# Optimization experiments

Hardware: AMD Instinct MI355X
Metric: run time of the kernel (lower is better)

## Reference

```python
import jax, jax.numpy as jnp
import numpy as np

B, N, D, H, R = 4, 4096, 1024, 16, 64
HD = D // H  # head_dim = 64


def setup_inputs() -> dict:
    key = jax.random.key(0)
    ks = jax.random.split(key, 8)
    x = jax.random.normal(ks[0], (B, N, D), dtype=jnp.float32)
    # nn.Linear weights are (out, in); y = x @ W.T
    Wq = jax.random.normal(ks[1], (D, D), dtype=jnp.float32) * (1.0 / np.sqrt(D))
    Wk = jax.random.normal(ks[2], (D, D), dtype=jnp.float32) * (1.0 / np.sqrt(D))
    Wv = jax.random.normal(ks[3], (D, D), dtype=jnp.float32) * (1.0 / np.sqrt(D))
    Wo = jax.random.normal(ks[4], (D, D), dtype=jnp.float32) * (1.0 / np.sqrt(D))
    bo = jnp.zeros((D,), dtype=jnp.float32)
    E = jax.random.normal(ks[5], (N, R), dtype=jnp.float32) * 0.02
    Fm = jax.random.normal(ks[6], (N, R), dtype=jnp.float32) * 0.02
    return {"x": x, "Wq": Wq, "Wk": Wk, "Wv": Wv, "Wo": Wo, "bo": bo, "E": E, "Fm": Fm}


def reference(x, Wq, Wk, Wv, Wo, bo, E, Fm):
    b, n, d = x.shape
    scale = np.sqrt(HD).astype(np.float32)
    # projections: torch Linear => x @ W.T ; reshape to (B, H, N, HD)
    def proj(W):
        y = jnp.einsum('bnd,ed->bne', x, W)
        return y.reshape(b, n, H, HD).transpose(0, 2, 1, 3)
    Q = proj(Wq)  # (B,H,N,HD)
    K = proj(Wk)
    V = proj(Wv)
    # low-rank projections along sequence: (B,H,R,HD)
    K_low = jnp.einsum('nr,bhnd->bhrd', E[:n], K)
    V_low = jnp.einsum('nr,bhnd->bhrd', Fm[:n], V)
    scores = jnp.einsum('bhnd,bhrd->bhnr', Q, K_low) / scale  # (B,H,N,R)
    attn = jax.nn.softmax(scores, axis=-1)
    out = jnp.einsum('bhnr,bhrd->bhnd', attn, V_low)  # (B,H,N,HD)
    out = out.transpose(0, 2, 1, 3).reshape(b, n, d)
    return jnp.einsum('bnd,ed->bne', out, Wo) + bo
```

## Files before the change

### kernel.cpp

```cpp
#include <hip/hip_runtime.h>
#include <stdint.h>

typedef __bf16 bf16;
typedef __bf16 bf16x8 __attribute__((ext_vector_type(8)));
typedef __bf16 bf16x4 __attribute__((ext_vector_type(4)));
typedef float  f32x4  __attribute__((ext_vector_type(4)));

#define NB   4096
#define DB   1024
#define RV   64
#define MB   16384
#define NSEG 8

__global__ void detect_dtype(const unsigned short* x, int* flag) {
  __shared__ int cnt;
  if (threadIdx.x == 0) cnt = 0;
  __syncthreads();
  int local = 0;
  for (int i = threadIdx.x; i < 8192; i += 256) {
    const int e = (x[i] >> 7) & 0xFF;
    if (e >= 0xC0) local++;
  }
  atomicAdd(&cnt, local);
  __syncthreads();
  if (threadIdx.x == 0) *flag = (cnt > 64) ? 1 : 0;
}

struct CvtArgs {
  const void* src[8];
  bf16* dst[8];
  int n[8];
  int off[9];
};
__global__ void to_bf16_multi(CvtArgs a, const int* __restrict__ flag) {
  const int blk = blockIdx.x;
  int seg = 0;
#pragma unroll
  for (int s = 1; s < 8; ++s) seg += (blk >= a.off[s]);
  const int i = (blk - a.off[seg]) * 2048 + threadIdx.x * 8;
  if (i >= a.n[seg]) return;
  bf16* dst = a.dst[seg];
  if (*flag) {
    const float* s = (const float*)a.src[seg] + i;
    f32x4 x0 = *(const f32x4*)s;
    f32x4 x1 = *(const f32x4*)(s + 4);
    bf16x8 v;
    v[0]=(bf16)x0[0]; v[1]=(bf16)x0[1]; v[2]=(bf16)x0[2]; v[3]=(bf16)x0[3];
    v[4]=(bf16)x1[0]; v[5]=(bf16)x1[1]; v[6]=(bf16)x1[2]; v[7]=(bf16)x1[3];
    *(bf16x8*)(dst + i) = v;
  } else {
    *(uint4*)(dst + i) = *(const uint4*)((const bf16*)a.src[seg] + i);
  }
}

__global__ __launch_bounds__(256) void ef_transpose(
    const void* __restrict__ E, const void* __restrict__ F,
    bf16* __restrict__ EFt, const int* __restrict__ flag) {
  const int m = blockIdx.x;
  const int z = m >> 6, r = m & 63;
  const void* src = z ? F : E;
  const int t = threadIdx.x;
  bf16* dst = EFt + (size_t)m * 4096;
  if (*flag) {
    const float* s = (const float*)src;
#pragma unroll
    for (int i = 0; i < 16; ++i) {
      const int n = i*256 + t;
      dst[n] = (bf16)s[(size_t)n*RV + r];
    }
  } else {
    const bf16* s = (const bf16*)src;
#pragma unroll
    for (int i = 0; i < 16; ++i) {
      const int n = i*256 + t;
      dst[n] = s[(size_t)n*RV + r];
    }
  }
}

typedef __attribute__((address_space(1))) const void g_as1_void;
typedef __attribute__((address_space(3))) void as3_void;
static __device__ __forceinline__ void gload16(const void* g, void* l) {
  __builtin_amdgcn_global_load_lds((g_as1_void*)g, (as3_void*)l, 16, 0, 0);
}

__global__ __launch_bounds__(256, 4) void lowrank_mfma(
    const bf16* __restrict__ EFt, const bf16* __restrict__ xb,
    float* __restrict__ Pf) {
  const int b = blockIdx.x, dt = blockIdx.y, seg = blockIdx.z;
  __shared__ __align__(16) bf16 sEF0[128*64];
  __shared__ __align__(16) bf16 sEF1[128*64];
  __shared__ __align__(16) bf16 sXT[32*64];
  const int t = threadIdx.x, lane = t & 63, w = t >> 6;
  const int lr = lane & 15, quad = lane >> 4;
  const int wm = (w & 1) * 64, wd = (w >> 1) * 16;
  const int nbase = seg * (NB / NSEG);

  const bf16* gA[4];
  int abase[4];
#pragma unroll
  for (int i = 0; i < 4; ++i) {
    const int c = i*256 + t, row = c >> 3, ch = c & 7;
    gA[i] = EFt + (size_t)row*4096 + nbase + (ch ^ (row & 7))*8;
    abase[i] = (i*256 + (w << 6)) * 8;
  }
  const bf16* gx = xb + ((size_t)b*NB + nbase + lane)*DB + dt*32 + w*8;
  int xslot[8];
#pragma unroll
  for (int j = 0; j < 8; ++j) {
    const int d = w*8 + j;
    xslot[j] = (d*8 + ((lane >> 3) ^ (d & 7)))*8 + (lane & 7);
  }
  f32x4 acc[4] = {};

  uint4 rx = *(const uint4*)gx;
#pragma unroll
  for (int i = 0; i < 4; ++i) gload16(gA[i], sEF0 + abase[i]);
  asm volatile("s_waitcnt vmcnt(0)" ::: "memory");
  __syncthreads();

  for (int kt = 0; kt < NB/NSEG; kt += 64) {
    {
      const bf16* px = (const bf16*)&rx;
#pragma unroll
      for (int j = 0; j < 8; ++j) sXT[xslot[j]] = px[j];
    }
    bf16* nbuf = ((kt >> 6) & 1) ? sEF0 : sEF1;
    if (kt + 64 < NB/NSEG) {
#pragma unroll
      for (int i = 0; i < 4; ++i) gload16(gA[i] + kt + 64, nbuf + abase[i]);
      rx = *(const uint4*)(gx + (size_t)(kt + 64)*DB);
    }
    asm volatile("s_waitcnt lgkmcnt(0)" ::: "memory");
    __syncthreads();
    const bf16* cbuf = ((kt >> 6) & 1) ? sEF1 : sEF0;
#pragma unroll
    for (int ks = 0; ks < 2; ++ks) {
      const int kc = ks*4 + quad;
      const int dd = wd + lr;
      bf16x8 bv = *(const bf16x8*)(sXT + (dd*8 + (kc ^ (dd & 7)))*8);
#pragma unroll
      for (int mi = 0; mi < 4; ++mi) {
        const int m = wm + mi*16 + lr;
        bf16x8 af = *(const bf16x8*)(cbuf + (m*8 + (kc ^ (m & 7)))*8);
        acc[mi] = __builtin_amdgcn_mfma_f32_16x16x32_bf16(af, bv, acc[mi], 0, 0, 0);
      }
    }
    if (kt + 64 < NB/NSEG) asm volatile("s_waitcnt vmcnt(1)" ::: "memory");
    __syncthreads();
  }

  float* dst = Pf + (((size_t)seg*4 + b)*128)*DB + dt*32 + wd + lr;
#pragma unroll
  for (int mi = 0; mi < 4; ++mi) {
    const int row128 = wm + mi*16 + quad*4;
#pragma unroll
    for (int rg = 0; rg < 4; ++rg)
      dst[(size_t)(row128 + rg)*DB] = acc[mi][rg];
  }
}

__global__ __launch_bounds__(256) void lowrank_reduce(
    const float* __restrict__ Pf, bf16* __restrict__ xEb, bf16* __restrict__ xFb) {
  const int idx = blockIdx.x*256 + threadIdx.x;
  const int d4  = idx & 255;
  const int row = (idx >> 8) & 127;
  const int b   = idx >> 15;
  const float* p = Pf + ((size_t)b*128 + row)*DB + d4*4;
  f32x4 s = {};
#pragma unroll
  for (int seg = 0; seg < NSEG; ++seg) {
    f32x4 v = *(const f32x4*)(p + (size_t)seg*4*128*DB);
    s[0]+=v[0]; s[1]+=v[1]; s[2]+=v[2]; s[3]+=v[3];
  }
  bf16x4 o;
  o[0]=(bf16)s[0]; o[1]=(bf16)s[1]; o[2]=(bf16)s[2]; o[3]=(bf16)s[3];
  bf16* dst = (row < 64 ? xEb : xFb) + ((size_t)b*64 + (row & 63))*DB + d4*4;
  *(bf16x4*)dst = o;
}

struct GemmArgs {
  const bf16* A;
  const bf16* B;
  void* C;
  const bf16* bias;
  const int* oflag;
  int force_f32;
  int M, N, K;
  const bf16* A2;
  const bf16* B2;
  void* C2;
  int dual;
};

__global__ __launch_bounds__(512, 2) void gemm_nt(GemmArgs args) {
  const int K = args.K, N = args.N;
  const bf16* Aptr = args.A;
  const bf16* Bptr = args.B;
  void* Cptr = args.C;
  __shared__ __align__(16) char smem[131072];
  bf16* const sA[4] = {(bf16*)smem,           (bf16*)(smem + 32768),
                       (bf16*)(smem + 65536), (bf16*)(smem + 98304)};
  bf16* const sB[4] = {(bf16*)(smem + 16384), (bf16*)(smem + 49152),
                       (bf16*)(smem + 81920), (bf16*)(smem + 114688)};

  const int t = threadIdx.x;
  const int lane = t & 63;
  const int w = t >> 6;
  const int lr = lane & 15;
  const int quad = lane >> 4;
  const int wm = (w >> 2) * 128;
  const int wn = (w & 3) * 64;

  int bx = blockIdx.x, by = blockIdx.y;
  if (args.dual) {
    if (by == 1) { Aptr = args.A2; Bptr = args.B2; Cptr = args.C2; }
    by = 0;
  } else if (gridDim.y == 64) {
    const int l = by * 4 + bx;
    const int xcd = l & 7, s = l >> 3;
    by = xcd * 8 + (s >> 2);
    bx = s & 3;
  }
  const int m0 = by * 256;
  const int n0 = bx * 256;

  const bf16* gA[2];
  const bf16* gB[2];
  int lds_off[2];
#pragma unroll
  for (int i = 0; i < 2; ++i) {
    const int c = i*512 + t, row = c >> 2, ch = c & 3;
    const int sc = ch ^ ((row >> 1) & 3);
    gA[i] = Aptr + (size_t)(m0 + row)*K + sc*8;
    gB[i] = Bptr + (size_t)(n0 + row)*K + sc*8;
    lds_off[i] = c * 8;
  }
  auto stage = [&](bf16* dA, bf16* dB, int ko) {
#pragma unroll
    for (int i = 0; i < 2; ++i) gload16(gA[i] + ko, dA + lds_off[i]);
#pragma unroll
    for (int i = 0; i < 2; ++i) gload16(gB[i] + ko, dB + lds_off[i]);
  };

  f32x4 acc[8][4] = {};

#define GSUB(J, WS, DOSTAGE) do {                                            \
    asm volatile("s_waitcnt " WS ::: "memory");                              \
    __builtin_amdgcn_s_barrier();                                            \
    bf16x8 af[8], bv[4];                                                     \
    _Pragma("unroll")                                                        \
    for (int mi = 0; mi < 8; ++mi) {                                         \
      const int m = wm + mi*16 + lr;                                         \
      af[mi] = *(const bf16x8*)(sA[J] + m*32 + ((quad ^ ((m>>1)&3))*8));     \
    }                                                                        \
    _Pragma("unroll")                                                        \
    for (int ni = 0; ni < 4; ++ni) {                                         \
      const int n = wn + ni*16 + lr;                                         \
      bv[ni] = *(const bf16x8*)(sB[J] + n*32 + ((quad ^ ((n>>1)&3))*8));     \
    }                                                                        \
    if (DOSTAGE) stage(sA[((J)+3)&3], sB[((J)+3)&3], kt + ((J)+3)*32);       \
    __builtin_amdgcn_s_setprio(1);                                           \
    _Pragma("unroll")                                                        \
    for (int mi = 0; mi < 8; ++mi)                                           \
      _Pragma("unroll")                                                      \
      for (int ni = 0; ni < 4; ++ni)                                         \
        acc[mi][ni] = __builtin_amdgcn_mfma_f32_16x16x32_bf16(               \
            af[mi], bv[ni], acc[mi][ni], 0, 0, 0);                           \
    __builtin_amdgcn_s_setprio(0);                                           \
  } while (0)

  stage(sA[0], sB[0], 0);
  stage(sA[1], sB[1], 32);
  stage(sA[2], sB[2], 64);

  int kt = 0;
  for (; kt + 128 < K; kt += 128) {
    GSUB(0, "vmcnt(8)", 1);
    GSUB(1, "vmcnt(8)", 1);
    GSUB(2, "vmcnt(8)", 1);
    GSUB(3, "vmcnt(8)", 1);
  }
  GSUB(0, "vmcnt(8)", 1);
  GSUB(1, "vmcnt(8)", 0);
  GSUB(2, "vmcnt(4)", 0);
  GSUB(3, "vmcnt(0)", 0);
#undef GSUB

  __syncthreads();

  const int f32out = args.force_f32 | (args.oflag ? *args.oflag : 0);
  float* sEw = (float*)(smem + w * 16384);
#pragma unroll
  for (int h = 0; h < 2; ++h) {
    if (h) asm volatile("s_waitcnt lgkmcnt(0)" ::: "memory");
#pragma unroll
    for (int mi = 0; mi < 4; ++mi) {
#pragma unroll
      for (int ni = 0; ni < 4; ++ni) {
        const int colg = n0 + wn + ni*16 + lr;
        const float bvv = args.bias ? (float)args.bias[colg] : 0.0f;
#pragma unroll
        for (int rg = 0; rg < 4; ++rg) {
          const int row = mi*16 + quad*4 + rg;
          sEw[row*64 + ((ni*16 + lr) ^ ((row & 15)*4))] = acc[h*4 + mi][ni][rg] + bvv;
        }
      }
    }
    asm volatile("s_waitcnt lgkmcnt(0)" ::: "memory");
#pragma unroll
    for (int i = 0; i < 8; ++i) {
      const int c = i*64 + lane;
      const int row = c >> 3, ch = c & 7;
      const int d0 = ch * 8;
      const int swz = (row & 15) * 4;
      f32x4 v0 = *(const f32x4*)(sEw + row*64 + (d0 ^ swz));
      f32x4 v1 = *(const f32x4*)(sEw + row*64 + ((d0 + 4) ^ swz));
      const size_t base = (size_t)(m0 + wm + h*64 + row)*N + n0 + wn + d0;
      if (f32out) {
        *(f32x4*)((float*)Cptr + base)     = v0;
        *(f32x4*)((float*)Cptr + base + 4) = v1;
      } else {
        bf16x8 wv;
        wv[0]=(bf16)v0[0]; wv[1]=(bf16)v0[1]; wv[2]=(bf16)v0[2]; wv[3]=(bf16)v0[3];
        wv[4]=(bf16)v1[0]; wv[5]=(bf16)v1[1]; wv[6]=(bf16)v1[2]; wv[7]=(bf16)v1[3];
        *(bf16x8*)((bf16*)Cptr + base) = wv;
      }
    }
  }
}

__global__ __launch_bounds__(256, 2) void attn_mfma(
    const bf16* Q, const float* __restrict__ Klow,
    const float* __restrict__ Vlow, bf16* AO) {
  const int bh = blockIdx.x, b = bh >> 4, h = bh & 15;
  const int n0 = blockIdx.y * 128;

  __shared__ bf16 sQ[128*64];
  __shared__ bf16 sKb[64*64];
  __shared__ bf16 sVt[64*64];
  __shared__ bf16 sP[4][32*64];

  const int t = threadIdx.x;
  const int lane = t & 63;
  const int w = t >> 6;
  const int lr = lane & 15;
  const int quad = lane >> 4;

#pragma unroll
  for (int i = 0; i < 4; ++i) {
    const int c = i*256 + t;
    const int row = c >> 3, j = c & 7;
    const uint4 v = *(const uint4*)(Q + ((size_t)b*NB + n0 + row)*DB + h*64 + j*8);
    *(uint4*)(sQ + (row*8 + (j ^ (row & 7)))*8) = v;
  }
  {
    const int r = t >> 2, c0 = (t & 3) * 16;
    const float* kb = Klow + (size_t)(b*64 + r)*DB + h*64 + c0;
    const float* vb = Vlow + (size_t)(b*64 + r)*DB + h*64 + c0;
    float kf[16], vf[16];
#pragma unroll
    for (int i = 0; i < 4; ++i) {
      *(f32x4*)(kf + i*4) = *(const f32x4*)(kb + i*4);
      *(f32x4*)(vf + i*4) = *(const f32x4*)(vb + i*4);
    }
#pragma unroll
    for (int cc = 0; cc < 2; ++cc) {
      bf16x8 pk;
#pragma unroll
      for (int j2 = 0; j2 < 8; ++j2) pk[j2] = (bf16)kf[cc*8 + j2];
      const int ch = (c0 >> 3) + cc;
      *(bf16x8*)(sKb + (r*8 + (ch ^ (r & 7)))*8) = pk;
    }
#pragma unroll
    for (int j2 = 0; j2 < 16; ++j2) {
      const int d = c0 + j2;
      sVt[d*64 + (((r >> 3) ^ (d & 7))*8) + (r & 7)] = (bf16)vf[j2];
    }
  }
  __syncthreads();

  f32x4 accS[2][4] = {};
#pragma unroll
  for (int ks = 0; ks < 2; ++ks) {
    const int kc = ks*4 + quad;
    bf16x8 af[2], bv[4];
#pragma unroll
    for (int mi = 0; mi < 2; ++mi) {
      const int m = w*32 + mi*16 + lr;
      af[mi] = *(const bf16x8*)(sQ + (m*8 + (kc ^ (m & 7)))*8);
    }
#pragma unroll
    for (int ni = 0; ni < 4; ++ni) {
      const int r = ni*16 + lr;
      bv[ni] = *(const bf16x8*)(sKb + (r*8 + (kc ^ (r & 7)))*8);
    }
#pragma unroll
    for (int mi = 0; mi < 2; ++mi)
#pragma unroll
      for (int ni = 0; ni < 4; ++ni)
        accS[mi][ni] = __builtin_amdgcn_mfma_f32_16x16x32_bf16(
            af[mi], bv[ni], accS[mi][ni], 0, 0, 0);
  }

  float inv_[2][4];
#pragma unroll
  for (int mi = 0; mi < 2; ++mi)
#pragma unroll
    for (int rg = 0; rg < 4; ++rg) {
      float mv = -3.0e38f;
#pragma unroll
      for (int ni = 0; ni < 4; ++ni) mv = fmaxf(mv, accS[mi][ni][rg]);
#pragma unroll
      for (int d = 1; d < 16; d <<= 1) mv = fmaxf(mv, __shfl_xor(mv, d));
      float sum = 0.0f;
#pragma unroll
      for (int ni = 0; ni < 4; ++ni) {
        const float p = __expf((accS[mi][ni][rg] - mv) * 0.125f);
        accS[mi][ni][rg] = p;
        sum += p;
      }
#pragma unroll
      for (int d = 1; d < 16; d <<= 1) sum += __shfl_xor(sum, d);
      inv_[mi][rg] = 1.0f / sum;
    }

  bf16* myP = sP[w];
#pragma unroll
  for (int mi = 0; mi < 2; ++mi)
#pragma unroll
    for (int ni = 0; ni < 4; ++ni)
#pragma unroll
      for (int rg = 0; rg < 4; ++rg) {
        const int row = mi*16 + quad*4 + rg;
        const int col = ni*16 + lr;
        myP[row*64 + ((col >> 3) ^ (row & 7))*8 + (col & 7)] = (bf16)accS[mi][ni][rg];
      }

  f32x4 accO[2][4] = {};
#pragma unroll
  for (int ks = 0; ks < 2; ++ks) {
    const int kc = ks*4 + quad;
    bf16x8 ap[2], bvv[4];
#pragma unroll
    for (int mi = 0; mi < 2; ++mi) {
      const int m = mi*16 + lr;
      ap[mi] = *(const bf16x8*)(myP + (m*8 + (kc ^ (m & 7)))*8);
    }
#pragma unroll
    for (int di = 0; di < 4; ++di) {
      const int d = di*16 + lr;
      bvv[di] = *(const bf16x8*)(sVt + (d*8 + (kc ^ (d & 7)))*8);
    }
#pragma unroll
    for (int mi = 0; mi < 2; ++mi)
#pragma unroll
      for (int di = 0; di < 4; ++di)
        accO[mi][di] = __builtin_amdgcn_mfma_f32_16x16x32_bf16(
            ap[mi], bvv[di], accO[mi][di], 0, 0, 0);
  }

#pragma unroll
  for (int mi = 0; mi < 2; ++mi)
#pragma unroll
    for (int di = 0; di < 4; ++di)
#pragma unroll
      for (int rg = 0; rg < 4; ++rg) {
        const int row = mi*16 + quad*4 + rg;
        const int col = di*16 + lr;
        myP[row*64 + ((col >> 3) ^ (row & 7))*8 + (col & 7)] =
            (bf16)(accO[mi][di][rg] * inv_[mi][rg]);
      }
  asm volatile("s_waitcnt lgkmcnt(0)" ::: "memory");
#pragma unroll
  for (int i = 0; i < 4; ++i) {
    const int c = i*64 + lane;
    const int row = c >> 3, ch = c & 7;
    const bf16x8 v = *(const bf16x8*)(myP + row*64 + ((ch ^ (row & 7))*8));
    *(bf16x8*)(AO + ((size_t)b*NB + n0 + w*32 + row)*DB + h*64 + ch*8) = v;
  }
}

extern "C" void kernel_launch(void* const* d_in, const int* in_sizes, int n_in,
                              void* d_out, int out_size, void* d_ws, size_t ws_size,
                              hipStream_t stream) {
  char* ws = (char*)d_ws;
  const size_t MiB = 1024*1024;
  int*   flag = (int*)ws;
  float* Klow = (float*)(ws + 1*MiB);
  float* Vlow = (float*)(ws + 2*MiB);
  bf16*  xEb  = (bf16*)(ws + 3*MiB);
  bf16*  xFb  = (bf16*)(ws + 3*MiB + 512*1024);
  bf16*  EFt  = (bf16*)(ws + 4*MiB);
  bf16*  Wqb  = (bf16*)(ws + 7*MiB);
  bf16*  Wkb  = (bf16*)(ws + 9*MiB);
  bf16*  Wvb  = (bf16*)(ws + 11*MiB);
  bf16*  Wob  = (bf16*)(ws + 13*MiB);
  bf16*  bob  = (bf16*)(ws + 15*MiB);
  bf16*  xb   = (bf16*)(ws + 20*MiB);
  bf16*  S0   = (bf16*)(ws + 52*MiB);
  float* Pf   = (float*)(ws + 52*MiB);

  detect_dtype<<<1, 256, 0, stream>>>((const unsigned short*)d_in[0], flag);

  ef_transpose<<<dim3(128), 256, 0, stream>>>(d_in[6], d_in[7], EFt, flag);

  CvtArgs ca;
  bf16* dsts[6] = {xb, Wqb, Wkb, Wvb, Wob, bob};
  int   ns[6]   = {16777216, 1048576, 1048576, 1048576, 1048576, 1024};
  int off = 0;
  for (int i = 0; i < 6; ++i) {
    ca.src[i] = d_in[i]; ca.dst[i] = dsts[i]; ca.n[i] = ns[i];
    ca.off[i] = off; off += (ns[i] + 2047) / 2048;
  }
  for (int i = 6; i < 8; ++i) {
    ca.src[i] = d_in[0]; ca.dst[i] = xb; ca.n[i] = 0; ca.off[i] = off;
  }
  ca.off[8] = off;
  to_bf16_multi<<<dim3(off), 256, 0, stream>>>(ca, flag);

  lowrank_mfma<<<dim3(4, 32, NSEG), 256, 0, stream>>>(EFt, xb, Pf);
  lowrank_reduce<<<dim3(512), 256, 0, stream>>>(Pf, xEb, xFb);

  GemmArgs ka;
  ka.A = xEb; ka.B = Wkb; ka.C = Klow;
  ka.A2 = xFb; ka.B2 = Wvb; ka.C2 = Vlow;
  ka.dual = 1;
  ka.bias = nullptr; ka.oflag = nullptr; ka.force_f32 = 1;
  ka.M = 256; ka.N = DB; ka.K = DB;
  gemm_nt<<<dim3(4, 2), 512, 0, stream>>>(ka);

  GemmArgs qa;
  qa.A = xb; qa.B = Wqb; qa.C = S0; qa.bias = nullptr;
  qa.oflag = nullptr; qa.force_f32 = 0;
  qa.A2 = nullptr; qa.B2 = nullptr; qa.C2 = nullptr; qa.dual = 0;
  qa.M = MB; qa.N = DB; qa.K = DB;
  gemm_nt<<<dim3(4, 64), 512, 0, stream>>>(qa);

  attn_mfma<<<dim3(64, 32), 256, 0, stream>>>(S0, Klow, Vlow, S0);

  GemmArgs oa;
  oa.A = S0; oa.B = Wob; oa.C = d_out; oa.bias = bob;
  oa.oflag = flag; oa.force_f32 = 0;
  oa.A2 = nullptr; oa.B2 = nullptr; oa.C2 = nullptr; oa.dual = 0;
  oa.M = MB; oa.N = DB; oa.K = DB;
  gemm_nt<<<dim3(4, 64), 512, 0, stream>>>(oa);
}
```

Before: 301.5 us.

## Replace 256x256 pipelined GEMM with simple 128x128 single-buffer tile kernel

Rewrites the bf16 NT GEMM from a 512-thread, 256x256 tile with a 4-stage LDS ring and manual vmcnt waits into a 256-thread, 128x128 tile with BK=64, single LDS buffer and two __syncthreads per k-step. It launches more blocks (1024 instead of 256 for the big GEMMs) at higher occupancy, and the dual low-rank GEMM now uses gridDim.z to pick its operands. The aim is better CU fill and latency hiding through occupancy. The cost is less operand reuse per block and no software pipelining of global loads against MFMA work.

Result: faster. 289.0 us (-4.1%).

```diff
diff --git a/kernel.cpp b/kernel.cpp
--- a/kernel.cpp
+++ b/kernel.cpp
@@ -193,130 +193,110 @@
   int dual;
 };
 
-__global__ __launch_bounds__(512, 2) void gemm_nt(GemmArgs args) {
+__global__ __launch_bounds__(256, 4) void gemm_nt(GemmArgs args) {
   const int K = args.K, N = args.N;
   const bf16* Aptr = args.A;
   const bf16* Bptr = args.B;
   void* Cptr = args.C;
-  __shared__ __align__(16) char smem[131072];
-  bf16* const sA[4] = {(bf16*)smem,           (bf16*)(smem + 32768),
-                       (bf16*)(smem + 65536), (bf16*)(smem + 98304)};
-  bf16* const sB[4] = {(bf16*)(smem + 16384), (bf16*)(smem + 49152),
-                       (bf16*)(smem + 81920), (bf16*)(smem + 114688)};
+  if (args.dual && blockIdx.z == 1) { Aptr = args.A2; Bptr = args.B2; Cptr = args.C2; }
+  __shared__ __align__(16) char smem[32768];
+  bf16* const sA = (bf16*)smem;
+  bf16* const sB = (bf16*)(smem + 16384);
 
   const int t = threadIdx.x;
   const int lane = t & 63;
   const int w = t >> 6;
   const int lr = lane & 15;
   const int quad = lane >> 4;
-  const int wm = (w >> 2) * 128;
-  const int wn = (w & 3) * 64;
+  const int wm = (w & 1) * 64;
+  const int wn = (w >> 1) * 64;
 
   int bx = blockIdx.x, by = blockIdx.y;
-  if (args.dual) {
-    if (by == 1) { Aptr = args.A2; Bptr = args.B2; Cptr = args.C2; }
-    by = 0;
-  } else if (gridDim.y == 64) {
-    const int l = by * 4 + bx;
+  if (gridDim.y == 128) {
+    const int l = by * 8 + bx;
     const int xcd = l & 7, s = l >> 3;
-    by = xcd * 8 + (s >> 2);
-    bx = s & 3;
-  }
-  const int m0 = by * 256;
-  const int n0 = bx * 256;
-
-  const bf16* gA[2];
-  const bf16* gB[2];
-  int lds_off[2];
-#pragma unroll
-  for (int i = 0; i < 2; ++i) {
-    const int c = i*512 + t, row = c >> 2, ch = c & 3;
-    const int sc = ch ^ ((row >> 1) & 3);
+    by = xcd * 16 + (s >> 3);
+    bx = s & 7;
+  }
+  const int m0 = by * 128;
+  const int n0 = bx * 128;
+
+  const bf16* gA[4];
+  const bf16* gB[4];
+  int lds_off[4];
+#pragma unroll
+  for (int i = 0; i < 4; ++i) {
+    const int c = i*256 + t;
+    const int row = c >> 3, ch = c & 7;
+    const int sc = ch ^ (row & 7);
     gA[i] = Aptr + (size_t)(m0 + row)*K + sc*8;
     gB[i] = Bptr + (size_t)(n0 + row)*K + sc*8;
-    lds_off[i] = c * 8;
-  }
-  auto stage = [&](bf16* dA, bf16* dB, int ko) {
-#pragma unroll
-    for (int i = 0; i < 2; ++i) gload16(gA[i] + ko, dA + lds_off[i]);
-#pragma unroll
-    for (int i = 0; i < 2; ++i) gload16(gB[i] + ko, dB + lds_off[i]);
-  };
-
-  f32x4 acc[8][4] = {};
-
-#define GSUB(J, WS, DOSTAGE) do {                                            \
-    asm volatile("s_waitcnt " WS ::: "memory");                              \
-    __builtin_amdgcn_s_barrier();                                            \
-    bf16x8 af[8], bv[4];                                                     \
-    _Pragma("unroll")                                                        \
-    for (int mi = 0; mi < 8; ++mi) {                                         \
-      const int m = wm + mi*16 + lr;                                         \
-      af[mi] = *(const bf16x8*)(sA[J] + m*32 + ((quad ^ ((m>>1)&3))*8));     \
-    }                                                                        \
-    _Pragma("unroll")                                                        \
-    for (int ni = 0; ni < 4; ++ni) {                                         \
-      const int n = wn + ni*16 + lr;                                         \
-      bv[ni] = *(const bf16x8*)(sB[J] + n*32 + ((quad ^ ((n>>1)&3))*8));     \
-    }                                                                        \
-    if (DOSTAGE) stage(sA[((J)+3)&3], sB[((J)+3)&3], kt + ((J)+3)*32);       \
-    __builtin_amdgcn_s_setprio(1);                                           \
-    _Pragma("unroll")                                                        \
-    for (int mi = 0; mi < 8; ++mi)                                           \
-      _Pragma("unroll")                                                      \
-      for (int ni = 0; ni < 4; ++ni)                                         \
-        acc[mi][ni] = __builtin_amdgcn_mfma_f32_16x16x32_bf16(               \
-            af[mi], bv[ni], acc[mi][ni], 0, 0, 0);                           \
-    __builtin_amdgcn_s_setprio(0);                                           \
-  } while (0)
-
-  stage(sA[0], sB[0], 0);
-  stage(sA[1], sB[1], 32);
-  stage(sA[2], sB[2], 64);
-
-  int kt = 0;
-  for (; kt + 128 < K; kt += 128) {
-    GSUB(0, "vmcnt(8)", 1);
-    GSUB(1, "vmcnt(8)", 1);
-    GSUB(2, "vmcnt(8)", 1);
-    GSUB(3, "vmcnt(8)", 1);
-  }
-  GSUB(0, "vmcnt(8)", 1);
-  GSUB(1, "vmcnt(8)", 0);
-  GSUB(2, "vmcnt(4)", 0);
-  GSUB(3, "vmcnt(0)", 0);
-#undef GSUB
+    lds_off[i] = (i*256 + w*64) * 8;
+  }
+
+  f32x4 acc[4][4] = {};
+
+  for (int kt = 0; kt < K; kt += 64) {
+    __syncthreads();
+#pragma unroll
+    for (int i = 0; i < 4; ++i) gload16(gA[i] + kt, sA + lds_off[i]);
+#pragma unroll
+    for (int i = 0; i < 4; ++i) gload16(gB[i] + kt, sB + lds_off[i]);
+    __syncthreads();
+#pragma unroll
+    for (int ks = 0; ks < 2; ++ks) {
+      const int kc = ks*4 + quad;
+      bf16x8 af[4], bv[4];
+#pragma unroll
+      for (int mi = 0; mi < 4; ++mi) {
+        const int m = wm + mi*16 + lr;
+        af[mi] = *(const bf16x8*)(sA + (m*8 + (kc ^ (m & 7)))*8);
+      }
+#pragma unroll
+      for (int ni = 0; ni < 4; ++ni) {
+        const int n = wn + ni*16 + lr;
+        bv[ni] = *(const bf16x8*)(sB + (n*8 + (kc ^ (n & 7)))*8);
+      }
+#pragma unroll
+      for (int mi = 0; mi < 4; ++mi)
+#pragma unroll
+        for (int ni = 0; ni < 4; ++ni)
+          acc[mi][ni] = __builtin_amdgcn_mfma_f32_16x16x32_bf16(
+              af[mi], bv[ni], acc[mi][ni], 0, 0, 0);
+    }
+  }
 
   __syncthreads();
 
   const int f32out = args.force_f32 | (args.oflag ? *args.oflag : 0);
-  float* sEw = (float*)(smem + w * 16384);
-#pragma unroll
-  for (int h = 0; h < 2; ++h) {
-    if (h) asm volatile("s_waitcnt lgkmcnt(0)" ::: "memory");
-#pragma unroll
-    for (int mi = 0; mi < 4; ++mi) {
+  float* sEw = (float*)(smem + w * 8192);
+#pragma unroll
+  for (int hh = 0; hh < 2; ++hh) {
+    if (hh) asm volatile("s_waitcnt lgkmcnt(0)" ::: "memory");
+#pragma unroll
+    for (int mi2 = 0; mi2 < 2; ++mi2) {
+      const int mi = hh*2 + mi2;
 #pragma unroll
       for (int ni = 0; ni < 4; ++ni) {
         const int colg = n0 + wn + ni*16 + lr;
         const float bvv = args.bias ? (float)args.bias[colg] : 0.0f;
 #pragma unroll
         for (int rg = 0; rg < 4; ++rg) {
-          const int row = mi*16 + quad*4 + rg;
-          sEw[row*64 + ((ni*16 + lr) ^ ((row & 15)*4))] = acc[h*4 + mi][ni][rg] + bvv;
+          const int row = mi2*16 + quad*4 + rg;
+          sEw[row*64 + ((ni*16 + lr) ^ ((row & 15)*4))] = acc[mi][ni][rg] + bvv;
         }
       }
     }
     asm volatile("s_waitcnt lgkmcnt(0)" ::: "memory");
 #pragma unroll
-    for (int i = 0; i < 8; ++i) {
+    for (int i = 0; i < 4; ++i) {
       const int c = i*64 + lane;
       const int row = c >> 3, ch = c & 7;
       const int d0 = ch * 8;
       const int swz = (row & 15) * 4;
       f32x4 v0 = *(const f32x4*)(sEw + row*64 + (d0 ^ swz));
       f32x4 v1 = *(const f32x4*)(sEw + row*64 + ((d0 + 4) ^ swz));
-      const size_t base = (size_t)(m0 + wm + h*64 + row)*N + n0 + wn + d0;
+      const size_t base = (size_t)(m0 + wm + hh*32 + row)*N + n0 + wn + d0;
       if (f32out) {
         *(f32x4*)((float*)Cptr + base)     = v0;
         *(f32x4*)((float*)Cptr + base + 4) = v1;
@@ -528,14 +508,14 @@
   ka.dual = 1;
   ka.bias = nullptr; ka.oflag = nullptr; ka.force_f32 = 1;
   ka.M = 256; ka.N = DB; ka.K = DB;
-  gemm_nt<<<dim3(4, 2), 512, 0, stream>>>(ka);
+  gemm_nt<<<dim3(8, 2, 2), 256, 0, stream>>>(ka);
 
   GemmArgs qa;
   qa.A = xb; qa.B = Wqb; qa.C = S0; qa.bias = nullptr;
   qa.oflag = nullptr; qa.force_f32 = 0;
   qa.A2 = nullptr; qa.B2 = nullptr; qa.C2 = nullptr; qa.dual = 0;
   qa.M = MB; qa.N = DB; qa.K = DB;
-  gemm_nt<<<dim3(4, 64), 512, 0, stream>>>(qa);
+  gemm_nt<<<dim3(8, 128, 1), 256, 0, stream>>>(qa);
 
   attn_mfma<<<dim3(64, 32), 256, 0, stream>>>(S0, Klow, Vlow, S0);
 
@@ -544,5 +524,5 @@
   oa.oflag = flag; oa.force_f32 = 0;
   oa.A2 = nullptr; oa.B2 = nullptr; oa.C2 = nullptr; oa.dual = 0;
   oa.M = MB; oa.N = DB; oa.K = DB;
-  gemm_nt<<<dim3(4, 64), 512, 0, stream>>>(oa);
-}
+  gemm_nt<<<dim3(8, 128, 1), 256, 0, stream>>>(oa);
+}
```
